# Performance work log

Hardware: AMD Instinct MI355X
Metric: run time of the kernel (lower is better)

The kernel has to match this reference:

```python
import jax, jax.numpy as jnp
import numpy as np

LATENT = 256
HIDDEN = 512
MAX_NODES = 64
TAU = 1.0
BATCH = 128
IDX_I, IDX_J = np.triu_indices(MAX_NODES, k=1)  # P = 2016 pairs
EPS = 1e-10


def fixed_positional_encoding(max_len, d_model):
    pos = np.arange(max_len)[:, None].astype(np.float32)
    div = np.exp(np.arange(0, d_model, 2).astype(np.float32) * (-np.log(10000.0) / d_model))
    pe = np.zeros((max_len, d_model), dtype=np.float32)
    pe[:, 0::2] = np.sin(pos * div)
    pe[:, 1::2] = np.cos(pos * div)
    return jnp.asarray(pe)


def setup_inputs() -> dict:
    key = jax.random.key(0)
    ks = jax.random.split(key, 20)

    def unif(k, shape, fan):
        bound = 1.0 / np.sqrt(fan)
        return jax.random.uniform(k, shape, jnp.float32, -bound, bound)

    inp = {}
    inp["z"] = jax.random.normal(ks[0], (BATCH, LATENT), jnp.float32)
    inp["n_nodes"] = jax.random.randint(ks[1], (BATCH,), 1, MAX_NODES + 1)  # lengths >= 1
    inp["n_edges"] = 100
    inp["gumbel_u"] = jax.random.uniform(ks[2], (BATCH, len(IDX_I), 2), jnp.float32)
    # learned params
    inp["emb"] = jax.random.normal(ks[3], (MAX_NODES, LATENT), jnp.float32)
    inp["pe"] = fixed_positional_encoding(MAX_NODES, LATENT)
    inp["W_pre"] = unif(ks[4], (LATENT, 2 * LATENT), 2 * LATENT)
    inp["b_pre"] = unif(ks[5], (LATENT,), 2 * LATENT)
    # GRU layer 0 (input LATENT) and layer 1 (input HIDDEN), torch layout [3H, in]/[3H, H]
    inp["Wih0"] = unif(ks[6], (3 * HIDDEN, LATENT), HIDDEN)
    inp["Whh0"] = unif(ks[7], (3 * HIDDEN, HIDDEN), HIDDEN)
    inp["bih0"] = unif(ks[8], (3 * HIDDEN,), HIDDEN)
    inp["bhh0"] = unif(ks[9], (3 * HIDDEN,), HIDDEN)
    inp["Wih1"] = unif(ks[10], (3 * HIDDEN, HIDDEN), HIDDEN)
    inp["Whh1"] = unif(ks[11], (3 * HIDDEN, HIDDEN), HIDDEN)
    inp["bih1"] = unif(ks[12], (3 * HIDDEN,), HIDDEN)
    inp["bhh1"] = unif(ks[13], (3 * HIDDEN,), HIDDEN)
    inp["node_W"] = unif(ks[14], (HIDDEN, HIDDEN), HIDDEN)
    inp["adj_W1"] = unif(ks[15], (HIDDEN, 2 * HIDDEN), 2 * HIDDEN)
    inp["adj_b1"] = unif(ks[16], (HIDDEN,), 2 * HIDDEN)
    inp["adj_W2"] = unif(ks[17], (2, HIDDEN), HIDDEN)
    inp["adj_b2"] = unif(ks[18], (2,), HIDDEN)
    return inp


def gru_layer(x, Wih, Whh, bih, bhh):
    # x: [B, T, D] -> outputs [B, T, H], torch GRU gate math
    xt = jnp.swapaxes(x, 0, 1)  # [T, B, D]
    gi_all = jnp.einsum("tbd,gd->tbg", xt, Wih) + bih  # precompute input gates
    H = Whh.shape[1]

    def step(h, gi):
        gh = h @ Whh.T + bhh
        ir, iz, inn = gi[:, :H], gi[:, H:2 * H], gi[:, 2 * H:]
        hr, hz, hn = gh[:, :H], gh[:, H:2 * H], gh[:, 2 * H:]
        r = jax.nn.sigmoid(ir + hr)
        zg = jax.nn.sigmoid(iz + hz)
        n = jnp.tanh(inn + r * hn)
        h_new = (1.0 - zg) * n + zg * h
        return h_new, h_new

    h0 = jnp.zeros((x.shape[0], H), x.dtype)
    _, ys = jax.lax.scan(step, h0, gi_all)
    return jnp.swapaxes(ys, 0, 1)  # [B, T, H]


def reference(z, n_nodes, n_edges, gumbel_u, emb, pe, W_pre, b_pre,
              Wih0, Whh0, bih0, bhh0, Wih1, Whh1, bih1, bhh1,
              node_W, adj_W1, adj_b1, adj_W2, adj_b2):
    B = z.shape[0]
    M = MAX_NODES
    # build RNN input: broadcast latent + sinusoidal PE, concat learned pos embedding
    seq = z[:, None, :] + pe[None]                              # [B, M, L]
    pos = jnp.broadcast_to(emb[None], (B, M, LATENT))           # [B, M, L]
    seq = jnp.concatenate([seq, pos], axis=-1)                  # [B, M, 2L]
    seq = seq @ W_pre.T + b_pre                                 # [B, M, L]
    mask = jnp.arange(M)[None, :] < n_nodes[:, None]            # [B, M]
    seq = seq * mask[:, :, None]
    # GRU (packed-sequence semantics == run full padded seq, zero padded outputs)
    h1 = gru_layer(seq, Wih0, Whh0, bih0, bhh0)
    rnn_out = gru_layer(h1, Wih1, Whh1, bih1, bhh1)
    rnn_out = rnn_out * mask[:, :, None]
    node_emb = rnn_out @ node_W.T                               # [B, M, H]
    # gather upper-triangle pairs -> MLP -> 2-way logits
    emb_i = node_emb[:, IDX_I, :]
    emb_j = node_emb[:, IDX_J, :]
    pair = jnp.concatenate([emb_i, emb_j], axis=-1)             # [B, P, 2H]
    hmid = jax.nn.relu(pair @ adj_W1.T + adj_b1)
    logits = hmid @ adj_W2.T + adj_b2                           # [B, P, 2]
    # gumbel-softmax, hard (straight-through)
    g = -jnp.log(-jnp.log(gumbel_u + EPS) + EPS)
    y_soft = jax.nn.softmax((logits + g) / TAU, axis=-1)
    y_hard = jax.nn.one_hot(jnp.argmax(y_soft, axis=-1), 2, dtype=y_soft.dtype)
    y = jax.lax.stop_gradient(y_hard - y_soft) + y_soft
    vals = y[..., 0]                                            # [B, P]
    # scatter into dense symmetric adjacency, mask by valid nodes
    adj = jnp.zeros((B, M, M), z.dtype).at[:, IDX_I, IDX_J].set(vals)
    adj = adj + jnp.swapaxes(adj, 1, 2)
    mask2d = (mask[:, :, None] & mask[:, None, :]).astype(adj.dtype)
    return adj * mask2d
```

## Files before the change

### kernel.cpp

```cpp
#include <hip/hip_runtime.h>
#include <math.h>

#define LATENT 256
#define HIDDEN 512
#define MAXN   64
#define BATCH  128
#define NPAIR  2016
#define G3     1536

#define HT_S   65536
#define GIT_S  196608
#define WT_S   1048576

__global__ __launch_bounds__(256) void pre_kernel(
    const float* __restrict__ z, const float* __restrict__ pe,
    const float* __restrict__ emb, const float* __restrict__ W_pre,
    const float* __restrict__ b_pre, float* __restrict__ ZC,
    float* __restrict__ adj,
    const float* __restrict__ adj_W1, const float* __restrict__ node_W,
    float* __restrict__ WAB,
    const float* __restrict__ Whh0, const float* __restrict__ Wih1,
    const float* __restrict__ Whh1, float* __restrict__ WT)
{
  __shared__ float s1[256];
  __shared__ float s2[256];
  int blk = blockIdx.x;
  int o = threadIdx.x;
  if (blk < 192) {
    int row = blk;
    if (row < 32) {
      int x = row * 256 + o;
      int b = x >> 6, d = x & 63;
      adj[(size_t)b * 4096 + d * 65] = 0.f;
    }
    const float* wr = W_pre + (size_t)o * 512;
    if (row < 128) {
      s1[o] = z[row * 256 + o];
      __syncthreads();
      float acc = 0.f;
      #pragma unroll 8
      for (int k = 0; k < 256; k += 4) {
        float4 w4 = *(const float4*)(wr + k);
        float4 x4 = *(const float4*)(&s1[k]);
        acc += x4.x * w4.x; acc += x4.y * w4.y; acc += x4.z * w4.z; acc += x4.w * w4.w;
      }
      ZC[row * 256 + o] = acc;
    } else {
      int m = row - 128;
      s1[o] = pe[m * 256 + o];
      s2[o] = emb[m * 256 + o];
      __syncthreads();
      float acc = b_pre[o];
      #pragma unroll 8
      for (int k = 0; k < 256; k += 4) {
        float4 w4 = *(const float4*)(wr + k);
        float4 x4 = *(const float4*)(&s1[k]);
        acc += x4.x * w4.x; acc += x4.y * w4.y; acc += x4.z * w4.z; acc += x4.w * w4.w;
      }
      #pragma unroll 8
      for (int k = 0; k < 256; k += 4) {
        float4 w4 = *(const float4*)(wr + 256 + k);
        float4 x4 = *(const float4*)(&s2[k]);
        acc += x4.x * w4.x; acc += x4.y * w4.y; acc += x4.z * w4.z; acc += x4.w * w4.w;
      }
      ZC[row * 256 + o] = acc;
    }
  } else if (blk < 448) {
    int idx = blk - 192;
    int k = (idx & 1) * 256 + o;
    int o0 = ((idx >> 1) & 63) * 8;
    int sel = idx >> 7;
    const float* a1 = adj_W1 + (sel ? 512 : 0);
    float acc[8] = {0.f, 0.f, 0.f, 0.f, 0.f, 0.f, 0.f, 0.f};
    for (int j = 0; j < 512; j++) {
      float w = node_W[(size_t)j * 512 + k];
      #pragma unroll
      for (int oo = 0; oo < 8; oo++)
        acc[oo] += a1[(size_t)(o0 + oo) * 1024 + j] * w;
    }
    #pragma unroll
    for (int oo = 0; oo < 8; oo++)
      WAB[(size_t)(sel * 512 + o0 + oo) * 512 + k] = acc[oo];
  } else {
    int idx2 = blk - 448;
    int mat = idx2 / 96;
    int r0 = (idx2 % 96) * 16;
    const float* Wsrc = (mat == 0) ? Whh0 : (mat == 1) ? Wih1 : Whh1;
    float* Wd = WT + (size_t)mat * WT_S;
    int r = r0 + (o >> 4);
    int oo = r & 511, g = r >> 9;
    int k0 = (o & 15) * 32;
    const float* src = Wsrc + (size_t)r * 512 + k0;
    for (int k = 0; k < 32; k++)
      Wd[((size_t)(k0 + k) * 512 + oo) * 4 + g] = src[k];
  }
}

template<bool MASK>
__global__ __launch_bounds__(256) void gemm_kernel(
    const float* __restrict__ A, int lda,
    const float* __restrict__ W, int ldw,
    const float* __restrict__ bias,
    float* __restrict__ C, int ldc,
    int M, int N, int K,
    const int* __restrict__ n_nodes)
{
  __shared__ float As[16][136];
  __shared__ float Ws[16][136];
  const int tid = threadIdx.x;
  const int tx = tid & 15, ty = tid >> 4;
  const int row0 = blockIdx.x * 128, col0 = blockIdx.y * 128;

  float acc[8][8];
  #pragma unroll
  for (int i = 0; i < 8; i++)
    #pragma unroll
    for (int j = 0; j < 8; j++) acc[i][j] = 0.f;

  float4 va[2], vw[2];
  auto load_tile = [&](int k0) {
    #pragma unroll
    for (int s = 0; s < 2; s++) {
      int q = tid + 256 * s;
      int r = q >> 2;
      int c4 = (q & 3) << 2;
      int gm = row0 + r;
      float4 v = make_float4(0.f, 0.f, 0.f, 0.f);
      if (gm < M) {
        v = *(const float4*)(A + (size_t)gm * lda + k0 + c4);
        if (MASK) {
          int bb = gm >> 6, tt = gm & 63;
          if (tt >= n_nodes[bb]) v = make_float4(0.f, 0.f, 0.f, 0.f);
        }
      }
      va[s] = v;
      int gn = col0 + r;
      vw[s] = *(const float4*)(W + (size_t)gn * ldw + k0 + c4);
    }
  };

  load_tile(0);
  for (int k0 = 0; k0 < K; k0 += 16) {
    __syncthreads();
    #pragma unroll
    for (int s = 0; s < 2; s++) {
      int q = tid + 256 * s;
      int r = q >> 2, c4 = (q & 3) << 2;
      As[c4 + 0][r] = va[s].x; As[c4 + 1][r] = va[s].y; As[c4 + 2][r] = va[s].z; As[c4 + 3][r] = va[s].w;
      Ws[c4 + 0][r] = vw[s].x; Ws[c4 + 1][r] = vw[s].y; Ws[c4 + 2][r] = vw[s].z; Ws[c4 + 3][r] = vw[s].w;
    }
    __syncthreads();
    if (k0 + 16 < K) load_tile(k0 + 16);
    #pragma unroll
    for (int kk = 0; kk < 16; kk++) {
      float4 a0 = *(const float4*)&As[kk][ty * 8];
      float4 a1 = *(const float4*)&As[kk][ty * 8 + 4];
      float4 b0 = *(const float4*)&Ws[kk][tx * 8];
      float4 b1 = *(const float4*)&Ws[kk][tx * 8 + 4];
      float av[8] = {a0.x, a0.y, a0.z, a0.w, a1.x, a1.y, a1.z, a1.w};
      float bv[8] = {b0.x, b0.y, b0.z, b0.w, b1.x, b1.y, b1.z, b1.w};
      #pragma unroll
      for (int i = 0; i < 8; i++)
        #pragma unroll
        for (int j = 0; j < 8; j++)
          acc[i][j] += av[i] * bv[j];
    }
  }

  float bb[8];
  #pragma unroll
  for (int j = 0; j < 8; j++) bb[j] = bias ? bias[col0 + tx * 8 + j] : 0.f;
  #pragma unroll
  for (int i = 0; i < 8; i++) {
    int gm = row0 + ty * 8 + i;
    if (gm < M) {
      float* out = C + (size_t)gm * ldc + col0 + tx * 8;
      float4 o0 = make_float4(acc[i][0] + bb[0], acc[i][1] + bb[1], acc[i][2] + bb[2], acc[i][3] + bb[3]);
      float4 o1 = make_float4(acc[i][4] + bb[4], acc[i][5] + bb[5], acc[i][6] + bb[6], acc[i][7] + bb[7]);
      *(float4*)out = o0;
      *(float4*)(out + 4) = o1;
    }
  }
}

__global__ __launch_bounds__(512) void gru_v5_kernel(
    const float* __restrict__ WT,
    const float* __restrict__ ZCW,
    const float* __restrict__ bih0, const float* __restrict__ bhh0,
    const float* __restrict__ bih1, const float* __restrict__ bhh1,
    const int* __restrict__ n_nodes,
    float* __restrict__ Ht1, float* __restrict__ GIt,
    float* __restrict__ H2t, float* __restrict__ H2row,
    int s)
{
  __shared__ float p_s[8][3][8][32];
  const int tid = threadIdx.x;
  const int plane = blockIdx.y;
  const int o0 = (blockIdx.x & 63) << 3;
  const int b0 = (blockIdx.x >> 6) << 5;

  int t; const float* Wmat; const float* Hin; bool dd;
  if (plane == 0)      { t = s;     Wmat = WT;            Hin = Ht1 + ((t - 1) & 1) * HT_S; dd = (t > 0); }
  else if (plane == 1) { t = s - 1; Wmat = WT + WT_S;     Hin = Ht1 + (t & 1) * HT_S;       dd = true; }
  else                 { t = s - 2; Wmat = WT + 2 * WT_S; Hin = H2t + ((t - 1) & 1) * HT_S; dd = (t > 0); }
  if (t < 0 || t > 63) return;

  float acc[3][4] = {{0.f, 0.f, 0.f, 0.f}, {0.f, 0.f, 0.f, 0.f}, {0.f, 0.f, 0.f, 0.f}};
  const int w = tid >> 6, l = tid & 63;
  const int bg = l & 7, rg = l >> 3;

  if (dd) {
    const float* hp_ = Hin + b0 + bg * 4 + (size_t)(w << 6) * 128;
    const float* wp_ = Wmat + (size_t)(o0 + rg) * 4 + (size_t)(w << 6) * 2048;
    #pragma unroll 4
    for (int k = 0; k < 64; k++) {
      float4 h4 = *(const float4*)(hp_ + (size_t)k * 128);
      float4 w4 = *(const float4*)(wp_ + (size_t)k * 2048);
      acc[0][0] += h4.x * w4.x; acc[0][1] += h4.y * w4.x; acc[0][2] += h4.z * w4.x; acc[0][3] += h4.w * w4.x;
      acc[1][0] += h4.x * w4.y; acc[1][1] += h4.y * w4.y; acc[1][2] += h4.z * w4.y; acc[1][3] += h4.w * w4.y;
      acc[2][0] += h4.x * w4.z; acc[2][1] += h4.y * w4.z; acc[2][2] += h4.z * w4.z; acc[2][3] += h4.w * w4.z;
    }
  }

  *(float4*)&p_s[w][0][rg][bg * 4] = make_float4(acc[0][0], acc[0][1], acc[0][2], acc[0][3]);
  *(float4*)&p_s[w][1][rg][bg * 4] = make_float4(acc[1][0], acc[1][1], acc[1][2], acc[1][3]);
  *(float4*)&p_s[w][2][rg][bg * 4] = make_float4(acc[2][0], acc[2][1], acc[2][2], acc[2][3]);
  __syncthreads();

  if (tid < 256) {
    int b = tid & 31, oi = tid >> 5;
    float s0 = 0.f, s1 = 0.f, s2 = 0.f;
    #pragma unroll
    for (int ww = 0; ww < 8; ww++) {
      s0 += p_s[ww][0][oi][b];
      s1 += p_s[ww][1][oi][b];
      s2 += p_s[ww][2][oi][b];
    }
    const int B = b0 + b, O = o0 + oi;

    if (plane == 0) {
      bool mk = t < n_nodes[B];
      float zr = mk ? ZCW[(size_t)B * G3 + O]        + ZCW[(size_t)(128 + t) * G3 + O]        : 0.f;
      float zz = mk ? ZCW[(size_t)B * G3 + 512 + O]  + ZCW[(size_t)(128 + t) * G3 + 512 + O]  : 0.f;
      float zn = mk ? ZCW[(size_t)B * G3 + 1024 + O] + ZCW[(size_t)(128 + t) * G3 + 1024 + O] : 0.f;
      float ir = zr + bih0[O], iz = zz + bih0[512 + O], inn = zn + bih0[1024 + O];
      float hr = s0 + bhh0[O], hz = s1 + bhh0[512 + O], hn = s2 + bhh0[1024 + O];
      float rg_ = 1.f / (1.f + expf(-(ir + hr)));
      float zg  = 1.f / (1.f + expf(-(iz + hz)));
      float ng  = tanhf(inn + rg_ * hn);
      float hp = (t > 0) ? Ht1[((t - 1) & 1) * HT_S + O * 128 + B] : 0.f;
      Ht1[(t & 1) * HT_S + O * 128 + B] = (1.f - zg) * ng + zg * hp;
    } else if (plane == 1) {
      size_t gb = (size_t)(t & 1) * GIT_S;
      GIt[gb + (size_t)O * 128 + B]          = s0 + bih1[O];
      GIt[gb + (size_t)(512 + O) * 128 + B]  = s1 + bih1[512 + O];
      GIt[gb + (size_t)(1024 + O) * 128 + B] = s2 + bih1[1024 + O];
    } else {
      size_t gb = (size_t)(t & 1) * GIT_S;
      float ir  = GIt[gb + (size_t)O * 128 + B];
      float iz  = GIt[gb + (size_t)(512 + O) * 128 + B];
      float inn = GIt[gb + (size_t)(1024 + O) * 128 + B];
      float hr = s0 + bhh1[O], hz = s1 + bhh1[512 + O], hn = s2 + bhh1[1024 + O];
      float rg_ = 1.f / (1.f + expf(-(ir + hr)));
      float zg  = 1.f / (1.f + expf(-(iz + hz)));
      float ng  = tanhf(inn + rg_ * hn);
      float hp = (t > 0) ? H2t[((t - 1) & 1) * HT_S + O * 128 + B] : 0.f;
      float hnew = (1.f - zg) * ng + zg * hp;
      H2t[(t & 1) * HT_S + O * 128 + B] = hnew;
      H2row[((size_t)(B * 64 + t)) * 512 + O] = hnew;
    }
  }
}

__global__ __launch_bounds__(256) void pair_kernel(
    const float* __restrict__ AB, const float* __restrict__ b1,
    const float* __restrict__ W2, const float* __restrict__ b2,
    const float* __restrict__ gu, const int* __restrict__ n_nodes,
    float* __restrict__ adj)
{
  int wid = blockIdx.x * 4 + (threadIdx.x >> 6);
  int lane = threadIdx.x & 63;
  int b = wid / NPAIR;
  int p = wid - b * NPAIR;

  float fp = (float)p;
  int i = (int)((127.0f - sqrtf(16129.0f - 8.0f * fp)) * 0.5f);
  if (i < 0) i = 0;
  if (i > 62) i = 62;
  while (i < 62 && (i + 1) * (126 - i) / 2 <= p) i++;
  while (i > 0 && i * (127 - i) / 2 > p) i--;
  int j = p - i * (127 - i) / 2 + i + 1;

  int n = n_nodes[b];
  if (i >= n || j >= n) {
    if (lane == 0) {
      adj[(size_t)b * 4096 + i * 64 + j] = 0.f;
      adj[(size_t)b * 4096 + j * 64 + i] = 0.f;
    }
    return;
  }

  const float* arow = AB + ((size_t)(b * 64 + i)) * 1024;
  const float* brow = AB + ((size_t)(b * 64 + j)) * 1024 + 512;
  int k0 = lane * 8;

  float4 a0 = *(const float4*)(arow + k0);
  float4 a1 = *(const float4*)(arow + k0 + 4);
  float4 q0 = *(const float4*)(brow + k0);
  float4 q1 = *(const float4*)(brow + k0 + 4);
  float4 c0 = *(const float4*)(b1 + k0);
  float4 c1 = *(const float4*)(b1 + k0 + 4);

  float h0 = fmaxf(a0.x + q0.x + c0.x, 0.f);
  float h1 = fmaxf(a0.y + q0.y + c0.y, 0.f);
  float h2 = fmaxf(a0.z + q0.z + c0.z, 0.f);
  float h3 = fmaxf(a0.w + q0.w + c0.w, 0.f);
  float h4 = fmaxf(a1.x + q1.x + c1.x, 0.f);
  float h5 = fmaxf(a1.y + q1.y + c1.y, 0.f);
  float h6 = fmaxf(a1.z + q1.z + c1.z, 0.f);
  float h7 = fmaxf(a1.w + q1.w + c1.w, 0.f);

  float4 w00 = *(const float4*)(W2 + k0);
  float4 w01 = *(const float4*)(W2 + k0 + 4);
  float4 w10 = *(const float4*)(W2 + 512 + k0);
  float4 w11 = *(const float4*)(W2 + 512 + k0 + 4);

  float acc0 = h0 * w00.x + h1 * w00.y + h2 * w00.z + h3 * w00.w
             + h4 * w01.x + h5 * w01.y + h6 * w01.z + h7 * w01.w;
  float acc1 = h0 * w10.x + h1 * w10.y + h2 * w10.z + h3 * w10.w
             + h4 * w11.x + h5 * w11.y + h6 * w11.z + h7 * w11.w;

  #pragma unroll
  for (int off = 32; off > 0; off >>= 1) {
    acc0 += __shfl_xor(acc0, off, 64);
    acc1 += __shfl_xor(acc1, off, 64);
  }

  if (lane == 0) {
    float s0 = acc0 + b2[0];
    float s1 = acc1 + b2[1];
    const float* u = gu + ((size_t)(b * NPAIR + p)) * 2;
    float g0 = -logf(-logf(u[0] + 1e-10f) + 1e-10f);
    float g1 = -logf(-logf(u[1] + 1e-10f) + 1e-10f);
    float val = ((s0 + g0) >= (s1 + g1)) ? 1.f : 0.f;
    adj[(size_t)b * 4096 + i * 64 + j] = val;
    adj[(size_t)b * 4096 + j * 64 + i] = val;
  }
}

extern "C" void kernel_launch(void* const* d_in, const int* in_sizes, int n_in,
                              void* d_out, int out_size, void* d_ws, size_t ws_size,
                              hipStream_t stream)
{
  (void)in_sizes; (void)n_in; (void)out_size; (void)ws_size;

  const float* z       = (const float*)d_in[0];
  const int*   n_nodes = (const int*)d_in[1];
  const float* gu      = (const float*)d_in[3];
  const float* emb     = (const float*)d_in[4];
  const float* pe      = (const float*)d_in[5];
  const float* W_pre   = (const float*)d_in[6];
  const float* b_pre   = (const float*)d_in[7];
  const float* Wih0    = (const float*)d_in[8];
  const float* Whh0    = (const float*)d_in[9];
  const float* bih0    = (const float*)d_in[10];
  const float* bhh0    = (const float*)d_in[11];
  const float* Wih1    = (const float*)d_in[12];
  const float* Whh1    = (const float*)d_in[13];
  const float* bih1    = (const float*)d_in[14];
  const float* bhh1    = (const float*)d_in[15];
  const float* node_W  = (const float*)d_in[16];
  const float* adj_W1  = (const float*)d_in[17];
  const float* adj_b1  = (const float*)d_in[18];
  const float* adj_W2  = (const float*)d_in[19];
  const float* adj_b2  = (const float*)d_in[20];
  float* adj = (float*)d_out;

  char* ws = (char*)d_ws;
  float* ZC    = (float*)(ws + 0);
  float* ZCW   = (float*)(ws + 196608);
  float* WAB   = (float*)(ws + 1376256);
  float* WT    = (float*)(ws + 3473408);
  float* Ht1   = (float*)(ws + 16056320);
  float* H2t   = (float*)(ws + 16580608);
  float* GIt   = (float*)(ws + 17104896);
  float* H2row = (float*)(ws + 18677760);
  float* AB    = (float*)(ws + 35454976);

  pre_kernel<<<736, 256, 0, stream>>>(z, pe, emb, W_pre, b_pre, ZC, adj,
                                      adj_W1, node_W, WAB,
                                      Whh0, Wih1, Whh1, WT);

  gemm_kernel<false><<<dim3(2, 12), 256, 0, stream>>>(
      ZC, 256, Wih0, 256, nullptr, ZCW, 1536, 192, 1536, 256, nullptr);

  for (int s = 0; s <= 65; s++)
    gru_v5_kernel<<<dim3(256, 3), 512, 0, stream>>>(
        WT, ZCW, bih0, bhh0, bih1, bhh1, n_nodes,
        Ht1, GIt, H2t, H2row, s);

  gemm_kernel<true><<<dim3(64, 8), 256, 0, stream>>>(
      H2row, 512, WAB, 512, nullptr, AB, 1024, 8192, 1024, 512, n_nodes);

  pair_kernel<<<64512, 256, 0, stream>>>(AB, adj_b1, adj_W2, adj_b2, gu, n_nodes, adj);
}
```

Measured before the change: 1.947 ms.

## Fuse layer-1 input projection into layer-1 recurrent GRU plane

The second GRU layer's input projection (Wih1·h1) moves out of its own plane and into the same block as the recurrent projection. Half the warps compute the input GEMV over 128 k-steps and the other half the hidden GEMV, then both are reduced separately in shared memory. This removes the GIt intermediate buffer and its global round trip, and shrinks the grid from three planes to two. The layer-0 hidden buffer becomes a 4-deep ring to cover the wider lag between stages, and each remaining warp now runs twice the k-loop length.

Measured after the change: 1.961 ms. No clear change (+0.7%).

```diff
diff --git a/kernel.cpp b/kernel.cpp
--- a/kernel.cpp
+++ b/kernel.cpp
@@ -9,7 +9,6 @@
 #define G3     1536
 
 #define HT_S   65536
-#define GIT_S  196608
 #define WT_S   1048576
 
 __global__ __launch_bounds__(256) void pre_kernel(
@@ -183,42 +182,60 @@
   }
 }
 
-__global__ __launch_bounds__(512) void gru_v5_kernel(
+__global__ __launch_bounds__(512) void gru_v8_kernel(
     const float* __restrict__ WT,
     const float* __restrict__ ZCW,
     const float* __restrict__ bih0, const float* __restrict__ bhh0,
     const float* __restrict__ bih1, const float* __restrict__ bhh1,
     const int* __restrict__ n_nodes,
-    float* __restrict__ Ht1, float* __restrict__ GIt,
-    float* __restrict__ H2t, float* __restrict__ H2row,
-    int s)
+    float* __restrict__ Ht1, float* __restrict__ H2t,
+    float* __restrict__ H2row, int s)
 {
   __shared__ float p_s[8][3][8][32];
   const int tid = threadIdx.x;
   const int plane = blockIdx.y;
   const int o0 = (blockIdx.x & 63) << 3;
   const int b0 = (blockIdx.x >> 6) << 5;
-
-  int t; const float* Wmat; const float* Hin; bool dd;
-  if (plane == 0)      { t = s;     Wmat = WT;            Hin = Ht1 + ((t - 1) & 1) * HT_S; dd = (t > 0); }
-  else if (plane == 1) { t = s - 1; Wmat = WT + WT_S;     Hin = Ht1 + (t & 1) * HT_S;       dd = true; }
-  else                 { t = s - 2; Wmat = WT + 2 * WT_S; Hin = H2t + ((t - 1) & 1) * HT_S; dd = (t > 0); }
-  if (t < 0 || t > 63) return;
-
-  float acc[3][4] = {{0.f, 0.f, 0.f, 0.f}, {0.f, 0.f, 0.f, 0.f}, {0.f, 0.f, 0.f, 0.f}};
   const int w = tid >> 6, l = tid & 63;
   const int bg = l & 7, rg = l >> 3;
 
-  if (dd) {
-    const float* hp_ = Hin + b0 + bg * 4 + (size_t)(w << 6) * 128;
-    const float* wp_ = Wmat + (size_t)(o0 + rg) * 4 + (size_t)(w << 6) * 2048;
-    #pragma unroll 4
-    for (int k = 0; k < 64; k++) {
-      float4 h4 = *(const float4*)(hp_ + (size_t)k * 128);
-      float4 w4 = *(const float4*)(wp_ + (size_t)k * 2048);
-      acc[0][0] += h4.x * w4.x; acc[0][1] += h4.y * w4.x; acc[0][2] += h4.z * w4.x; acc[0][3] += h4.w * w4.x;
-      acc[1][0] += h4.x * w4.y; acc[1][1] += h4.y * w4.y; acc[1][2] += h4.z * w4.y; acc[1][3] += h4.w * w4.y;
-      acc[2][0] += h4.x * w4.z; acc[2][1] += h4.y * w4.z; acc[2][2] += h4.z * w4.z; acc[2][3] += h4.w * w4.z;
+  int t;
+  if (plane == 0) { t = s;     if (t > 63) return; }
+  else            { t = s - 2; if (t < 0)  return; }
+
+  float acc[3][4] = {{0.f, 0.f, 0.f, 0.f}, {0.f, 0.f, 0.f, 0.f}, {0.f, 0.f, 0.f, 0.f}};
+
+  if (plane == 0) {
+    if (t > 0) {
+      const float* hp_ = Ht1 + ((t - 1) & 3) * HT_S + b0 + bg * 4 + (size_t)(w << 6) * 128;
+      const float* wp_ = WT + (size_t)(o0 + rg) * 4 + (size_t)(w << 6) * 2048;
+      #pragma unroll 8
+      for (int k = 0; k < 64; k++) {
+        float4 h4 = *(const float4*)(hp_ + (size_t)k * 128);
+        float4 w4 = *(const float4*)(wp_ + (size_t)k * 2048);
+        acc[0][0] += h4.x * w4.x; acc[0][1] += h4.y * w4.x; acc[0][2] += h4.z * w4.x; acc[0][3] += h4.w * w4.x;
+        acc[1][0] += h4.x * w4.y; acc[1][1] += h4.y * w4.y; acc[1][2] += h4.z * w4.y; acc[1][3] += h4.w * w4.y;
+        acc[2][0] += h4.x * w4.z; acc[2][1] += h4.y * w4.z; acc[2][2] += h4.z * w4.z; acc[2][3] += h4.w * w4.z;
+      }
+    }
+  } else {
+    const bool isIn = (w < 4);
+    const bool run = isIn || (t > 0);
+    if (run) {
+      const int kb = (w & 3) << 7;
+      const float* Wm = isIn ? (WT + WT_S) : (WT + 2 * WT_S);
+      const float* Hi = isIn ? (Ht1 + (t & 3) * HT_S)
+                             : (H2t + ((t - 1) & 1) * HT_S);
+      const float* hp_ = Hi + b0 + bg * 4 + (size_t)kb * 128;
+      const float* wp_ = Wm + (size_t)(o0 + rg) * 4 + (size_t)kb * 2048;
+      #pragma unroll 8
+      for (int k = 0; k < 128; k++) {
+        float4 h4 = *(const float4*)(hp_ + (size_t)k * 128);
+        float4 w4 = *(const float4*)(wp_ + (size_t)k * 2048);
+        acc[0][0] += h4.x * w4.x; acc[0][1] += h4.y * w4.x; acc[0][2] += h4.z * w4.x; acc[0][3] += h4.w * w4.x;
+        acc[1][0] += h4.x * w4.y; acc[1][1] += h4.y * w4.y; acc[1][2] += h4.z * w4.y; acc[1][3] += h4.w * w4.y;
+        acc[2][0] += h4.x * w4.z; acc[2][1] += h4.y * w4.z; acc[2][2] += h4.z * w4.z; acc[2][3] += h4.w * w4.z;
+      }
     }
   }
 
@@ -229,16 +246,16 @@
 
   if (tid < 256) {
     int b = tid & 31, oi = tid >> 5;
-    float s0 = 0.f, s1 = 0.f, s2 = 0.f;
-    #pragma unroll
-    for (int ww = 0; ww < 8; ww++) {
-      s0 += p_s[ww][0][oi][b];
-      s1 += p_s[ww][1][oi][b];
-      s2 += p_s[ww][2][oi][b];
-    }
     const int B = b0 + b, O = o0 + oi;
 
     if (plane == 0) {
+      float s0 = 0.f, s1 = 0.f, s2 = 0.f;
+      #pragma unroll
+      for (int ww = 0; ww < 8; ww++) {
+        s0 += p_s[ww][0][oi][b];
+        s1 += p_s[ww][1][oi][b];
+        s2 += p_s[ww][2][oi][b];
+      }
       bool mk = t < n_nodes[B];
       float zr = mk ? ZCW[(size_t)B * G3 + O]        + ZCW[(size_t)(128 + t) * G3 + O]        : 0.f;
       float zz = mk ? ZCW[(size_t)B * G3 + 512 + O]  + ZCW[(size_t)(128 + t) * G3 + 512 + O]  : 0.f;
@@ -248,19 +265,24 @@
       float rg_ = 1.f / (1.f + expf(-(ir + hr)));
       float zg  = 1.f / (1.f + expf(-(iz + hz)));
       float ng  = tanhf(inn + rg_ * hn);
-      float hp = (t > 0) ? Ht1[((t - 1) & 1) * HT_S + O * 128 + B] : 0.f;
-      Ht1[(t & 1) * HT_S + O * 128 + B] = (1.f - zg) * ng + zg * hp;
-    } else if (plane == 1) {
-      size_t gb = (size_t)(t & 1) * GIT_S;
-      GIt[gb + (size_t)O * 128 + B]          = s0 + bih1[O];
-      GIt[gb + (size_t)(512 + O) * 128 + B]  = s1 + bih1[512 + O];
-      GIt[gb + (size_t)(1024 + O) * 128 + B] = s2 + bih1[1024 + O];
+      float hp = (t > 0) ? Ht1[((t - 1) & 3) * HT_S + O * 128 + B] : 0.f;
+      Ht1[(t & 3) * HT_S + O * 128 + B] = (1.f - zg) * ng + zg * hp;
     } else {
-      size_t gb = (size_t)(t & 1) * GIT_S;
-      float ir  = GIt[gb + (size_t)O * 128 + B];
-      float iz  = GIt[gb + (size_t)(512 + O) * 128 + B];
-      float inn = GIt[gb + (size_t)(1024 + O) * 128 + B];
-      float hr = s0 + bhh1[O], hz = s1 + bhh1[512 + O], hn = s2 + bhh1[1024 + O];
+      float gi0 = 0.f, gi1 = 0.f, gi2 = 0.f, gh0 = 0.f, gh1 = 0.f, gh2 = 0.f;
+      #pragma unroll
+      for (int ww = 0; ww < 4; ww++) {
+        gi0 += p_s[ww][0][oi][b];
+        gi1 += p_s[ww][1][oi][b];
+        gi2 += p_s[ww][2][oi][b];
+      }
+      #pragma unroll
+      for (int ww = 4; ww < 8; ww++) {
+        gh0 += p_s[ww][0][oi][b];
+        gh1 += p_s[ww][1][oi][b];
+        gh2 += p_s[ww][2][oi][b];
+      }
+      float ir = gi0 + bih1[O], iz = gi1 + bih1[512 + O], inn = gi2 + bih1[1024 + O];
+      float hr = gh0 + bhh1[O], hz = gh1 + bhh1[512 + O], hn = gh2 + bhh1[1024 + O];
       float rg_ = 1.f / (1.f + expf(-(ir + hr)));
       float zg  = 1.f / (1.f + expf(-(iz + hz)));
       float ng  = tanhf(inn + rg_ * hn);
@@ -382,10 +404,9 @@
   float* WAB   = (float*)(ws + 1376256);
   float* WT    = (float*)(ws + 3473408);
   float* Ht1   = (float*)(ws + 16056320);
-  float* H2t   = (float*)(ws + 16580608);
-  float* GIt   = (float*)(ws + 17104896);
-  float* H2row = (float*)(ws + 18677760);
-  float* AB    = (float*)(ws + 35454976);
+  float* H2t   = (float*)(ws + 17104896);
+  float* H2row = (float*)(ws + 17629184);
+  float* AB    = (float*)(ws + 34406400);
 
   pre_kernel<<<736, 256, 0, stream>>>(z, pe, emb, W_pre, b_pre, ZC, adj,
                                       adj_W1, node_W, WAB,
@@ -395,9 +416,9 @@
       ZC, 256, Wih0, 256, nullptr, ZCW, 1536, 192, 1536, 256, nullptr);
 
   for (int s = 0; s <= 65; s++)
-    gru_v5_kernel<<<dim3(256, 3), 512, 0, stream>>>(
+    gru_v8_kernel<<<dim3(256, 2), 512, 0, stream>>>(
         WT, ZCW, bih0, bhh0, bih1, bhh1, n_nodes,
-        Ht1, GIt, H2t, H2row, s);
+        Ht1, H2t, H2row, s);
 
   gemm_kernel<true><<<dim3(64, 8), 256, 0, stream>>>(
       H2row, 512, WAB, 512, nullptr, AB, 1024, 8192, 1024, 512, n_nodes);
```
